# Kernel optimization log

Measured on AMD Instinct MI355X. Metric: run time of the kernel, lower is better.

Reference implementation:

```python
import jax, jax.numpy as jnp
import numpy as np

K = 60           # output_size (num tags)
START_TAG = 58
STOP_TAG = 59
NEG = -10000.0


def _conv1d(x, w, b, pad):
    # x: (B, Cin, T), w: (Cout, Cin, k) -> (B, Cout, T)
    y = jax.lax.conv_general_dilated(x, w, (1,), [(pad, pad)],
                                     dimension_numbers=('NCH', 'OIH', 'NCH'))
    return y + b[None, :, None]


def _cnn_feats(sentence, w1, b1, w2, b2, w3, b3, w4, b4, w5, b5, fc_w, fc_b):
    # sentence: (T, B, 3) -> (B, 3, T)
    x = jnp.transpose(sentence, (1, 2, 0))
    in2 = jax.nn.relu(_conv1d(x, w1, b1, 1))
    in3 = jax.nn.relu(_conv1d(in2, w2, b2, 1))
    in4 = jax.nn.relu(_conv1d(in3 + in2, w3, b3, 1))
    in5 = jax.nn.relu(_conv1d(in4 + in3, w4, b4, 1))
    c5 = jax.nn.relu(_conv1d(in5 + in4, w5, b5, 2))
    h = jnp.transpose(c5, (2, 0, 1))                 # (T, B, H)
    return jnp.einsum('tbh,kh->tbk', h, fc_w) + fc_b  # (T, B, K)


def _viterbi(feats, trans):
    Bsz = feats.shape[1]
    fv0 = jnp.full((Bsz, K), NEG, dtype=feats.dtype).at[:, START_TAG].set(0.0)

    def step(fv, feat):
        # scores[b, next, prev] = fv[b, prev] + trans[next, prev]
        scores = fv[:, None, :] + trans[None, :, :]
        bptr = jnp.argmax(scores, axis=2)             # (B, K)
        fv_new = jnp.max(scores, axis=2) + feat       # (B, K)
        return fv_new, bptr

    fv, bptrs = jax.lax.scan(step, fv0, feats)        # bptrs: (T, B, K)
    terminal = fv + trans[STOP_TAG]                   # (B, K)
    path_score = jnp.max(terminal, axis=1)            # (B,)
    best_last = jnp.argmax(terminal, axis=1)          # (B,)

    def back(tag, bp):
        prev = jnp.take_along_axis(bp, tag[:, None], axis=1)[:, 0]
        return prev, tag

    _, best_path = jax.lax.scan(back, best_last, bptrs, reverse=True)  # (T, B)
    return path_score, best_path


def setup_inputs() -> dict:
    key = jax.random.key(0)
    ks = jax.random.split(key, 14)
    T, B, HID = 8192, 2, 512

    def u(k, shape, fan_in):
        bound = 1.0 / np.sqrt(fan_in).astype(np.float32)
        return jax.random.uniform(k, shape, minval=-bound, maxval=bound, dtype=jnp.float32)

    sentence = jax.random.normal(ks[0], (T, B, 3), dtype=jnp.float32)
    w1 = u(ks[1], (HID, 3, 3), 3 * 3);      b1 = u(ks[2], (HID,), 3 * 3)
    w2 = u(ks[3], (HID, HID, 3), HID * 3);  b2 = u(ks[4], (HID,), HID * 3)
    w3 = u(ks[5], (HID, HID, 3), HID * 3);  b3 = u(ks[6], (HID,), HID * 3)
    w4 = u(ks[7], (HID, HID, 3), HID * 3);  b4 = u(ks[8], (HID,), HID * 3)
    w5 = u(ks[9], (HID, HID, 5), HID * 5);  b5 = u(ks[10], (HID,), HID * 5)
    fc_w = u(ks[11], (K, HID), HID);        fc_b = u(ks[12], (K,), HID)

    trans = jax.random.normal(ks[13], (K, K), dtype=jnp.float32)
    m = np.zeros((K, K), dtype=bool)
    m[START_TAG, :] = True
    m[:, STOP_TAG] = True
    for i in range(2, K):
        for j in range(2, K):
            if j <= i or j >= i + 2:
                m[j, i] = True
    trans = jnp.where(jnp.asarray(m), jnp.float32(NEG), trans)

    return {'sentence': sentence,
            'w1': w1, 'b1': b1, 'w2': w2, 'b2': b2, 'w3': w3, 'b3': b3,
            'w4': w4, 'b4': b4, 'w5': w5, 'b5': b5,
            'fc_w': fc_w, 'fc_b': fc_b, 'trans': trans}


def reference(sentence, w1, b1, w2, b2, w3, b3, w4, b4, w5, b5, fc_w, fc_b, trans):
    feats = _cnn_feats(sentence, w1, b1, w2, b2, w3, b3, w4, b4, w5, b5, fc_w, fc_b)
    path_score, best_path = _viterbi(feats, trans)
    return path_score, best_path
```

## Files before the change

kernel.cpp:

```cpp
#include <hip/hip_runtime.h>

#define BATCH 2
#define HID 512
#define KTAGS 60
#define NEGV -10000.0f
#define NINF -3.0e38f

template<int CTRL>
__device__ __forceinline__ float dmax(float x) {
    int r = __builtin_amdgcn_update_dpp(__float_as_int(x), __float_as_int(x),
                                        CTRL, 0xf, 0xf, false);
    return fmaxf(x, __int_as_float(r));
}
template<int CTRL>
__device__ __forceinline__ float dmov(float x, float old) {
    int r = __builtin_amdgcn_update_dpp(__float_as_int(old), __float_as_int(x),
                                        CTRL, 0xf, 0xf, false);
    return __int_as_float(r);
}
template<int L>
__device__ __forceinline__ float rdl(float x) {
    return __int_as_float(__builtin_amdgcn_readlane(__float_as_int(x), L));
}

__global__ __launch_bounds__(256) void conv1_kernel(
    const float* __restrict__ sent, const float* __restrict__ w1,
    const float* __restrict__ b1, float* __restrict__ y, int T, int B)
{
    int t = blockIdx.x * 256 + threadIdx.x;
    int c = blockIdx.y;
    int b = blockIdx.z;
    if (t >= T) return;
    float acc = b1[c];
#pragma unroll
    for (int dk = 0; dk < 3; ++dk) {
        int tt = t + dk - 1;
        if (tt >= 0 && tt < T) {
#pragma unroll
            for (int ci = 0; ci < 3; ++ci)
                acc += sent[(size_t)tt * (B * 3) + b * 3 + ci] * w1[c * 9 + ci * 3 + dk];
        }
    }
    y[((size_t)b * HID + c) * T + t] = fmaxf(acc, 0.f);
}

__global__ __launch_bounds__(256) void wtrans_kernel(
    const float* __restrict__ w, float* __restrict__ wt, int K)
{
    int idx = blockIdx.x * 256 + threadIdx.x;
    int total = HID * HID * K;
    if (idx >= total) return;
    int co = idx / (HID * K);
    int rem = idx % (HID * K);
    int ci = rem / K, dk = rem % K;
    wt[((size_t)ci * K + dk) * HID + co] = w[idx];
}

template<int KTAP, bool RES>
__global__ __launch_bounds__(256) void conv_kernel(
    const float* __restrict__ x1, const float* __restrict__ x2,
    const float* __restrict__ wt, const float* __restrict__ bias,
    float* __restrict__ y, int T)
{
    const int PAD = KTAP / 2;
    const int t0 = blockIdx.x * 64;
    const int co0 = blockIdx.y * 128;
    const int b = blockIdx.z;
    __shared__ float Xs[16][72];
    __shared__ float Ws[16][KTAP][128];
    const int tid = threadIdx.x;
    const int tx = tid & 15;
    const int ty = tid >> 4;
    float acc[8][4] = {};
    const size_t plane = (size_t)HID * T;
    const float* xa = x1 + (size_t)b * plane;
    const float* xb = RES ? (x2 + (size_t)b * plane) : nullptr;

    for (int c0 = 0; c0 < HID; c0 += 16) {
        for (int i = tid; i < 16 * 68; i += 256) {
            int ci = i / 68, tt = i % 68;
            int t = t0 + tt - 2;
            float v = 0.f;
            if (t >= 0 && t < T) {
                size_t off = (size_t)(c0 + ci) * T + t;
                v = xa[off];
                if (RES) v += xb[off];
            }
            Xs[ci][tt] = v;
        }
        for (int i = tid; i < 16 * KTAP * 32; i += 256) {
            int c4 = i & 31;
            int r = i >> 5;
            int dk = r % KTAP, ci = r / KTAP;
            *(float4*)&Ws[ci][dk][c4 * 4] =
                *(const float4*)&wt[(((size_t)(c0 + ci) * KTAP + dk) * HID) + co0 + c4 * 4];
        }
        __syncthreads();
#pragma unroll 4
        for (int ci = 0; ci < 16; ++ci) {
            float f8[8];
            *(float4*)&f8[0] = *(const float4*)&Xs[ci][tx * 4];
            *(float4*)&f8[4] = *(const float4*)&Xs[ci][tx * 4 + 4];
#pragma unroll
            for (int dk = 0; dk < KTAP; ++dk) {
                float wv[8];
                *(float4*)&wv[0] = *(const float4*)&Ws[ci][dk][ty * 8];
                *(float4*)&wv[4] = *(const float4*)&Ws[ci][dk][ty * 8 + 4];
#pragma unroll
                for (int r = 0; r < 8; ++r)
#pragma unroll
                    for (int c = 0; c < 4; ++c)
                        acc[r][c] = fmaf(wv[r], f8[c + dk + (2 - PAD)], acc[r][c]);
            }
        }
        __syncthreads();
    }
#pragma unroll
    for (int r = 0; r < 8; ++r) {
        int co = co0 + ty * 8 + r;
        float bv = bias[co];
#pragma unroll
        for (int c = 0; c < 4; ++c) {
            int t = t0 + tx * 4 + c;
            float v = acc[r][c] + bv;
            y[(size_t)b * plane + (size_t)co * T + t] = fmaxf(v, 0.f);
        }
    }
}

__global__ __launch_bounds__(256) void fc_kernel(
    const float* __restrict__ x, const float* __restrict__ fw,
    const float* __restrict__ fb, float* __restrict__ feats, int T)
{
    int t0 = blockIdx.x * 64, b = blockIdx.y;
    __shared__ float Xs[64][65];
    __shared__ float Ws[64][60];
    int tid = threadIdx.x;
    int k = tid & 63, tq = tid >> 6;
    float acc[16] = {};
    const float* xb = x + (size_t)b * HID * T;
    for (int c0 = 0; c0 < HID; c0 += 64) {
        for (int i = tid; i < 64 * 64; i += 256) {
            int ci = i >> 6, tt = i & 63;
            Xs[ci][tt] = xb[(size_t)(c0 + ci) * T + t0 + tt];
        }
        for (int i = tid; i < 64 * 60; i += 256) {
            int kk = i % 60, ci = i / 60;
            Ws[ci][kk] = fw[(size_t)kk * HID + c0 + ci];
        }
        __syncthreads();
        if (k < KTAGS) {
#pragma unroll 8
            for (int ci = 0; ci < 64; ++ci) {
                float wv = Ws[ci][k];
#pragma unroll
                for (int i = 0; i < 16; ++i)
                    acc[i] = fmaf(wv, Xs[ci][tq * 16 + i], acc[i]);
            }
        }
        __syncthreads();
    }
    float bv = (k < KTAGS) ? fb[k] : 0.f;
#pragma unroll
    for (int i = 0; i < 16; ++i) {
        int t = t0 + tq * 16 + i;
        feats[((size_t)t * 2 + b) * 64 + k] = (k < KTAGS) ? acc[i] + bv : NINF;
    }
}

__global__ __launch_bounds__(64) void viterbi_fwd(
    const float* __restrict__ feats, const float* __restrict__ trans,
    float* __restrict__ fvbuf, int T)
{
    const int b = blockIdx.x;
    const int l = threadIdx.x;
    if (l >= 16) return;
    float tc0[4], tc1[4], trc[4], tr0[4], tr1[4], fv[4];
#pragma unroll
    for (int j = 0; j < 4; ++j) {
        int k = 4 * l + j;
        int kc = (k < KTAGS) ? k : (KTAGS - 1);
        bool real = (k < KTAGS);
        tc0[j] = trans[kc * KTAGS + 0];
        tc1[j] = trans[kc * KTAGS + 1];
        trc[j] = (kc >= 1) ? trans[kc * KTAGS + (kc - 1)] : NINF;
        tr0[j] = real ? trans[0 * KTAGS + kc] : NINF;
        tr1[j] = real ? trans[1 * KTAGS + kc] : NINF;
        fv[j]  = real ? ((k == 58) ? 0.f : NEGV) : NINF;
    }
    {
        float4 st = {fv[0], fv[1], fv[2], fv[3]};
        *(float4*)&fvbuf[(size_t)b * 64 + 4 * l] = st;
    }
    const float* fp = feats + b * 64 + 4 * l;
    float* fvp = fvbuf + 128 + b * 64 + 4 * l;

    auto step = [&](float4 f, int j, float* outp) {
        float a0 = fmaxf(fmaxf(fv[0] + tr0[0], fv[1] + tr0[1]), fmaxf(fv[2] + tr0[2], fv[3] + tr0[3]));
        float a1 = fmaxf(fmaxf(fv[0] + tr1[0], fv[1] + tr1[1]), fmaxf(fv[2] + tr1[2], fv[3] + tr1[3]));
        float hi = fmaxf(fv[2], fv[3]);
        float m2 = (l == 0) ? hi : fmaxf(fmaxf(fv[0], fv[1]), hi);
        a0 = dmax<0x111>(a0); a0 = dmax<0x112>(a0); a0 = dmax<0x114>(a0); a0 = dmax<0x118>(a0);
        a1 = dmax<0x111>(a1); a1 = dmax<0x112>(a1); a1 = dmax<0x114>(a1); a1 = dmax<0x118>(a1);
        m2 = dmax<0x111>(m2); m2 = dmax<0x112>(m2); m2 = dmax<0x114>(m2); m2 = dmax<0x118>(m2);
        float R0 = rdl<14>(a0), R1 = rdl<14>(a1), M2 = rdl<14>(m2);
        float fv0s = rdl<0>(fv[0]);
        float fv1s = rdl<0>(fv[1]);
        float p3 = dmov<0x111>(fv[3], fv[3]);
        float bulk = M2 + NEGV;
        float o0 = fv[0], o1 = fv[1], o2 = fv[2];
        float g0 = fmaxf(fmaxf(fv0s + tc0[0], fv1s + tc1[0]), fmaxf(p3 + trc[0], bulk)) + f.x;
        float g1 = fmaxf(fmaxf(fv0s + tc0[1], fv1s + tc1[1]), fmaxf(o0 + trc[1], bulk)) + f.y;
        float g2 = fmaxf(fmaxf(fv0s + tc0[2], fv1s + tc1[2]), fmaxf(o1 + trc[2], bulk)) + f.z;
        float g3 = fmaxf(fmaxf(fv0s + tc0[3], fv1s + tc1[3]), fmaxf(o2 + trc[3], bulk)) + f.w;
        fv[0] = (l == 0) ? (R0 + f.x) : g0;
        fv[1] = (l == 0) ? (R1 + f.y) : g1;
        fv[2] = g2;
        fv[3] = g3;
        float4 st = {fv[0], fv[1], fv[2], fv[3]};
        *(float4*)&outp[j * 128] = st;
    };

    float4 fr[8];
#pragma unroll
    for (int j = 0; j < 8; ++j) fr[j] = *(const float4*)&fp[j * 128];
    fp += 8 * 128;

    for (int t = 0; t < T; t += 8) {
#pragma unroll
        for (int j = 0; j < 8; ++j) {
            step(fr[j], j, fvp);
            fr[j] = *(const float4*)&fp[j * 128];
        }
        fp += 8 * 128;
        fvp += 8 * 128;
    }
}

__global__ __launch_bounds__(256) void bptr_kernel(
    const float* __restrict__ fvbuf, const float* __restrict__ trans,
    unsigned char* __restrict__ bp, int T)
{
    int b = blockIdx.y;
    int t0 = blockIdx.x * 16;
    __shared__ float trT[KTAGS][64];
    __shared__ float fvs[16][64];
    int tid = threadIdx.x;
    for (int i = tid; i < KTAGS * 64; i += 256) {
        int p = i >> 6, nx = i & 63;
        trT[p][nx] = (nx < KTAGS) ? trans[(size_t)nx * KTAGS + p] : NINF;
    }
    for (int i = tid; i < 16 * 64; i += 256) {
        int w = i >> 6, lx = i & 63;
        fvs[w][lx] = fvbuf[((size_t)(t0 + w) * 2 + b) * 64 + lx];
    }
    __syncthreads();
    int nx = tid & 63, w0 = tid >> 6;
    if (nx < KTAGS) {
#pragma unroll
        for (int j = 0; j < 4; ++j) {
            int w = w0 * 4 + j;
            float m = NINF; int am = 0;
            for (int p = 0; p < KTAGS; ++p) {
                float s = fvs[w][p] + trT[p][nx];
                if (s > m) { m = s; am = p; }
            }
            bp[((size_t)(t0 + w) * 2 + b) * 64 + nx] = (unsigned char)am;
        }
    }
}

__global__ __launch_bounds__(64) void vit_chunkmap(
    const unsigned char* __restrict__ bp, unsigned char* __restrict__ cmap)
{
    int c = blockIdx.x, b = blockIdx.y;
    __shared__ unsigned char bl[128][64];
    int tid = threadIdx.x;
    const unsigned int* src = (const unsigned int*)bp;
    for (int i = tid; i < 128 * 16; i += 64) {
        int row = i >> 4, q = i & 15;
        ((unsigned int*)&bl[row][0])[q] = src[((size_t)(c * 128 + row) * 2 + b) * 16 + q];
    }
    __syncthreads();
    if (tid < KTAGS) {
        int tag = tid;
#pragma unroll 1
        for (int i = 127; i >= 0; --i) tag = bl[i][tag];
        cmap[(c * 2 + b) * 64 + tid] = (unsigned char)tag;
    }
}

__global__ void vit_boundary(const unsigned char* __restrict__ cmap,
                             const float* __restrict__ fvbuf,
                             const float* __restrict__ trans,
                             int* __restrict__ xbound, float* __restrict__ out,
                             int nch, int T)
{
    int b = threadIdx.x;
    if (b < BATCH) {
        const float* fvT = fvbuf + ((size_t)T * 2 + b) * 64;
        float m = NINF; int am = 0;
        for (int p = 0; p < KTAGS; ++p) {
            float s = fvT[p] + trans[59 * KTAGS + p];
            if (s > m) { m = s; am = p; }
        }
        out[b] = m;
        int tag = am;
        for (int c = nch - 1; c >= 0; --c) {
            xbound[c * 2 + b] = tag;
            tag = cmap[(c * 2 + b) * 64 + tag];
        }
    }
}

__global__ __launch_bounds__(64) void vit_emit(
    const unsigned char* __restrict__ bp, const int* __restrict__ xbound,
    float* __restrict__ out)
{
    int c = blockIdx.x, b = blockIdx.y;
    __shared__ unsigned char bl[128][64];
    int tid = threadIdx.x;
    const unsigned int* src = (const unsigned int*)bp;
    for (int i = tid; i < 128 * 16; i += 64) {
        int row = i >> 4, q = i & 15;
        ((unsigned int*)&bl[row][0])[q] = src[((size_t)(c * 128 + row) * 2 + b) * 16 + q];
    }
    __syncthreads();
    if (tid == 0) {
        int tag = xbound[c * 2 + b];
        for (int i = 127; i >= 0; --i) {
            out[2 + (size_t)(c * 128 + i) * 2 + b] = (float)tag;
            tag = bl[i][tag];
        }
    }
}

extern "C" void kernel_launch(void* const* d_in, const int* in_sizes, int n_in,
                              void* d_out, int out_size, void* d_ws, size_t ws_size,
                              hipStream_t stream) {
    const float* sent = (const float*)d_in[0];
    const float* w1 = (const float*)d_in[1];  const float* b1 = (const float*)d_in[2];
    const float* w2 = (const float*)d_in[3];  const float* b2 = (const float*)d_in[4];
    const float* w3 = (const float*)d_in[5];  const float* b3 = (const float*)d_in[6];
    const float* w4 = (const float*)d_in[7];  const float* b4 = (const float*)d_in[8];
    const float* w5 = (const float*)d_in[9];  const float* b5 = (const float*)d_in[10];
    const float* fw = (const float*)d_in[11]; const float* fb = (const float*)d_in[12];
    const float* trans = (const float*)d_in[13];

    const int B = BATCH;
    const int T = in_sizes[0] / (B * 3);

    char* ws = (char*)d_ws;
    const size_t SZBUF = (size_t)2 * HID * 8192 * 4;
    float* bufA = (float*)(ws);
    float* bufB = (float*)(ws + SZBUF);
    float* bufC = (float*)(ws + 2 * SZBUF);
    float* wslot = (float*)(ws + 3 * SZBUF);
    float* feats = wslot;
    float* fvbuf = bufC;
    unsigned char* bp = (unsigned char*)ws;
    unsigned char* cmap = (unsigned char*)(ws + 2 * 1024 * 1024);
    int* xbound = (int*)(ws + 3 * 1024 * 1024);
    float* outp = (float*)d_out;

    conv1_kernel<<<dim3(T / 256, HID, B), 256, 0, stream>>>(sent, w1, b1, bufA, T, B);

    wtrans_kernel<<<(HID * HID * 3 + 255) / 256, 256, 0, stream>>>(w2, wslot, 3);
    conv_kernel<3, false><<<dim3(T / 64, HID / 128, B), 256, 0, stream>>>(bufA, nullptr, wslot, b2, bufB, T);
    wtrans_kernel<<<(HID * HID * 3 + 255) / 256, 256, 0, stream>>>(w3, wslot, 3);
    conv_kernel<3, true ><<<dim3(T / 64, HID / 128, B), 256, 0, stream>>>(bufB, bufA, wslot, b3, bufC, T);
    wtrans_kernel<<<(HID * HID * 3 + 255) / 256, 256, 0, stream>>>(w4, wslot, 3);
    conv_kernel<3, true ><<<dim3(T / 64, HID / 128, B), 256, 0, stream>>>(bufC, bufB, wslot, b4, bufA, T);
    wtrans_kernel<<<(HID * HID * 5 + 255) / 256, 256, 0, stream>>>(w5, wslot, 5);
    conv_kernel<5, true ><<<dim3(T / 64, HID / 128, B), 256, 0, stream>>>(bufA, bufC, wslot, b5, bufB, T);

    fc_kernel<<<dim3(T / 64, B), 256, 0, stream>>>(bufB, fw, fb, feats, T);

    viterbi_fwd<<<dim3(B), 64, 0, stream>>>(feats, trans, fvbuf, T);
    bptr_kernel<<<dim3(T / 16, B), 256, 0, stream>>>(fvbuf, trans, bp, T);
    vit_chunkmap<<<dim3(T / 128, B), 64, 0, stream>>>(bp, cmap);
    vit_boundary<<<dim3(1), 64, 0, stream>>>(cmap, fvbuf, trans, xbound, outp, T / 128, T);
    vit_emit<<<dim3(T / 128, B), 64, 0, stream>>>(bp, xbound, outp);
}
```

Baseline: 4.451 ms.

## Register-prefetch conv tiles and use butterfly DPP reductions in Viterbi scan

```diff
diff --git a/kernel.cpp b/kernel.cpp
--- a/kernel.cpp
+++ b/kernel.cpp
@@ -18,9 +18,12 @@
                                         CTRL, 0xf, 0xf, false);
     return __int_as_float(r);
 }
-template<int L>
-__device__ __forceinline__ float rdl(float x) {
-    return __int_as_float(__builtin_amdgcn_readlane(__float_as_int(x), L));
+__device__ __forceinline__ float bfly16max(float x) {
+    x = dmax<0xB1>(x);
+    x = dmax<0x4E>(x);
+    x = dmax<0x141>(x);
+    x = dmax<0x140>(x);
+    return x;
 }
 
 __global__ __launch_bounds__(256) void conv1_kernel(
@@ -76,26 +79,56 @@
     const float* xa = x1 + (size_t)b * plane;
     const float* xb = RES ? (x2 + (size_t)b * plane) : nullptr;
 
+    float xr[5];
+    float4 wr[2 * KTAP];
+    int xci[5], xtt[5];
+#pragma unroll
+    for (int k = 0; k < 5; ++k) {
+        int i = tid + k * 256;
+        xci[k] = i / 68;
+        xtt[k] = i % 68;
+    }
+
+    auto load_stage = [&](int c0) {
+#pragma unroll
+        for (int k = 0; k < 5; ++k) {
+            float v = 0.f;
+            if (tid + k * 256 < 16 * 68) {
+                int t = t0 + xtt[k] - 2;
+                if (t >= 0 && t < T) {
+                    size_t off = (size_t)(c0 + xci[k]) * T + t;
+                    v = xa[off];
+                    if (RES) v += xb[off];
+                }
+            }
+            xr[k] = v;
+        }
+#pragma unroll
+        for (int k = 0; k < 2 * KTAP; ++k) {
+            int i = tid + k * 256;
+            int c4 = i & 31, r = i >> 5;
+            int dk = r % KTAP, ci = r / KTAP;
+            wr[k] = *(const float4*)&wt[(((size_t)(c0 + ci) * KTAP + dk) * HID) + co0 + c4 * 4];
+        }
+    };
+    auto write_stage = [&]() {
+#pragma unroll
+        for (int k = 0; k < 5; ++k)
+            if (tid + k * 256 < 16 * 68) Xs[xci[k]][xtt[k]] = xr[k];
+#pragma unroll
+        for (int k = 0; k < 2 * KTAP; ++k) {
+            int i = tid + k * 256;
+            int c4 = i & 31, r = i >> 5;
+            int dk = r % KTAP, ci = r / KTAP;
+            *(float4*)&Ws[ci][dk][c4 * 4] = wr[k];
+        }
+    };
+
+    load_stage(0);
     for (int c0 = 0; c0 < HID; c0 += 16) {
-        for (int i = tid; i < 16 * 68; i += 256) {
-            int ci = i / 68, tt = i % 68;
-            int t = t0 + tt - 2;
-            float v = 0.f;
-            if (t >= 0 && t < T) {
-                size_t off = (size_t)(c0 + ci) * T + t;
-                v = xa[off];
-                if (RES) v += xb[off];
-            }
-            Xs[ci][tt] = v;
-        }
-        for (int i = tid; i < 16 * KTAP * 32; i += 256) {
-            int c4 = i & 31;
-            int r = i >> 5;
-            int dk = r % KTAP, ci = r / KTAP;
-            *(float4*)&Ws[ci][dk][c4 * 4] =
-                *(const float4*)&wt[(((size_t)(c0 + ci) * KTAP + dk) * HID) + co0 + c4 * 4];
-        }
+        write_stage();
         __syncthreads();
+        if (c0 + 16 < HID) load_stage(c0 + 16);
 #pragma unroll 4
         for (int ci = 0; ci < 16; ++ci) {
             float f8[8];
@@ -188,51 +221,57 @@
         tr1[j] = real ? trans[1 * KTAGS + kc] : NINF;
         fv[j]  = real ? ((k == 58) ? 0.f : NEGV) : NINF;
     }
+    float fv0h = NEGV, fv1h = NEGV;
     {
         float4 st = {fv[0], fv[1], fv[2], fv[3]};
         *(float4*)&fvbuf[(size_t)b * 64 + 4 * l] = st;
     }
-    const float* fp = feats + b * 64 + 4 * l;
+    const float* fp   = feats + b * 64 + 4 * l;
+    const float* fp01 = feats + b * 64;
     float* fvp = fvbuf + 128 + b * 64 + 4 * l;
 
-    auto step = [&](float4 f, int j, float* outp) {
+    auto step = [&](float4 f, float2 f01, int j, float* outp) {
         float a0 = fmaxf(fmaxf(fv[0] + tr0[0], fv[1] + tr0[1]), fmaxf(fv[2] + tr0[2], fv[3] + tr0[3]));
         float a1 = fmaxf(fmaxf(fv[0] + tr1[0], fv[1] + tr1[1]), fmaxf(fv[2] + tr1[2], fv[3] + tr1[3]));
         float hi = fmaxf(fv[2], fv[3]);
         float m2 = (l == 0) ? hi : fmaxf(fmaxf(fv[0], fv[1]), hi);
-        a0 = dmax<0x111>(a0); a0 = dmax<0x112>(a0); a0 = dmax<0x114>(a0); a0 = dmax<0x118>(a0);
-        a1 = dmax<0x111>(a1); a1 = dmax<0x112>(a1); a1 = dmax<0x114>(a1); a1 = dmax<0x118>(a1);
-        m2 = dmax<0x111>(m2); m2 = dmax<0x112>(m2); m2 = dmax<0x114>(m2); m2 = dmax<0x118>(m2);
-        float R0 = rdl<14>(a0), R1 = rdl<14>(a1), M2 = rdl<14>(m2);
-        float fv0s = rdl<0>(fv[0]);
-        float fv1s = rdl<0>(fv[1]);
+        a0 = bfly16max(a0);
+        a1 = bfly16max(a1);
+        m2 = bfly16max(m2);
         float p3 = dmov<0x111>(fv[3], fv[3]);
-        float bulk = M2 + NEGV;
-        float o0 = fv[0], o1 = fv[1], o2 = fv[2];
-        float g0 = fmaxf(fmaxf(fv0s + tc0[0], fv1s + tc1[0]), fmaxf(p3 + trc[0], bulk)) + f.x;
-        float g1 = fmaxf(fmaxf(fv0s + tc0[1], fv1s + tc1[1]), fmaxf(o0 + trc[1], bulk)) + f.y;
-        float g2 = fmaxf(fmaxf(fv0s + tc0[2], fv1s + tc1[2]), fmaxf(o1 + trc[2], bulk)) + f.z;
-        float g3 = fmaxf(fmaxf(fv0s + tc0[3], fv1s + tc1[3]), fmaxf(o2 + trc[3], bulk)) + f.w;
-        fv[0] = (l == 0) ? (R0 + f.x) : g0;
-        fv[1] = (l == 0) ? (R1 + f.y) : g1;
+        float bulk = m2 + NEGV;
+        float nf0 = a0 + f01.x;
+        float nf1 = a1 + f01.y;
+        float g0 = fmaxf(fmaxf(fv0h + tc0[0], fv1h + tc1[0]), fmaxf(p3    + trc[0], bulk)) + f.x;
+        float g1 = fmaxf(fmaxf(fv0h + tc0[1], fv1h + tc1[1]), fmaxf(fv[0] + trc[1], bulk)) + f.y;
+        float g2 = fmaxf(fmaxf(fv0h + tc0[2], fv1h + tc1[2]), fmaxf(fv[1] + trc[2], bulk)) + f.z;
+        float g3 = fmaxf(fmaxf(fv0h + tc0[3], fv1h + tc1[3]), fmaxf(fv[2] + trc[3], bulk)) + f.w;
+        fv[0] = (l == 0) ? nf0 : g0;
+        fv[1] = (l == 0) ? nf1 : g1;
         fv[2] = g2;
         fv[3] = g3;
+        fv0h = nf0; fv1h = nf1;
         float4 st = {fv[0], fv[1], fv[2], fv[3]};
         *(float4*)&outp[j * 128] = st;
     };
 
     float4 fr[8];
-#pragma unroll
-    for (int j = 0; j < 8; ++j) fr[j] = *(const float4*)&fp[j * 128];
-    fp += 8 * 128;
+    float2 fr2[8];
+#pragma unroll
+    for (int j = 0; j < 8; ++j) {
+        fr[j]  = *(const float4*)&fp[j * 128];
+        fr2[j] = *(const float2*)&fp01[j * 128];
+    }
+    fp += 8 * 128; fp01 += 8 * 128;
 
     for (int t = 0; t < T; t += 8) {
 #pragma unroll
         for (int j = 0; j < 8; ++j) {
-            step(fr[j], j, fvp);
-            fr[j] = *(const float4*)&fp[j * 128];
-        }
-        fp += 8 * 128;
+            step(fr[j], fr2[j], j, fvp);
+            fr[j]  = *(const float4*)&fp[j * 128];
+            fr2[j] = *(const float2*)&fp01[j * 128];
+        }
+        fp += 8 * 128; fp01 += 8 * 128;
         fvp += 8 * 128;
     }
 }
```

After: 4.183 ms. 6.0% less time.
